# Kernel optimization log

Measured on AMD Instinct MI355X. Metric: run time of the kernel, lower is better.

Reference implementation:

```python
import jax, jax.numpy as jnp
import numpy as np

N = 8192          # num_points
RADIUS = 0.5


def _make_curve(num_points):
    # Reproduces the interp1d-based turbo-coil curve from __init__ (linear interp).
    xk = np.array([-2, -1, 0, 1, 1, 0, -1, -1, 0, 1, 2], dtype=np.float64)
    zk = np.array([0, 0, 1, 0, -1, 0, 1, 0, -1, 0, 0], dtype=np.float64)
    yk = np.array([0, 0, 1, 1, -1, -1, -1, 1, 1, 0, 0], dtype=np.float64)
    t = np.linspace(0.0, 1.0, len(xk))
    s = np.linspace(0.0, 1.0, num_points)
    return (np.interp(s, t, xk).astype(np.float32),
            np.interp(s, t, yk).astype(np.float32),
            np.interp(s, t, zk).astype(np.float32))


def setup_inputs() -> dict:
    x, y, z = _make_curve(N)
    return {"x": jnp.asarray(x), "y": jnp.asarray(y), "z": jnp.asarray(z)}


def _cdist(a, b):
    # pairwise Euclidean distance, safe at zero (subgradient 0 like torch.cdist)
    d2 = jnp.sum(a * a, -1, keepdims=True) - 2.0 * (a @ b.T) + jnp.sum(b * b, -1)
    d2 = jnp.maximum(d2, 0.0)
    safe = jnp.where(d2 > 0.0, d2, 1.0)
    return jnp.where(d2 > 0.0, jnp.sqrt(safe), 0.0)


def _mask_distances(dist, min_dist):
    # Original: for each row i, scan j = i, i+1, ... and overwrite entries with
    # min_dist+1 while dist[i,j] <= min_dist, breaking at the first entry that
    # exceeds min_dist (the j in range(i,0) loop is empty, so only the forward
    # scan matters). Vectorized: contiguous prefix-run starting at the diagonal.
    n = dist.shape[0]
    rows = jnp.arange(n)[:, None]
    cols = jnp.arange(n)[None, :]
    upper = cols >= rows
    cond = dist <= min_dist
    # cumprod along each row, seeded with 1 (True) left of the diagonal, so that
    # run[i,j] = all(cond[i, i..j]) for j >= i
    run = jnp.cumprod(jnp.where(upper, cond, True).astype(jnp.int32), axis=1)
    mask = upper & (run > 0)
    return jnp.where(mask, min_dist + 1.0, dist)


def _puffer_loss(p2d, low, high):
    # PufferZone(points_2d, -1.0, 1.0, x): out-of-bounds penalty on [low, high]
    return jax.nn.relu(p2d - high) + jax.nn.relu(low - p2d)


def _noise_loss(p2d):
    # noise_reduction_loss: penalize curvature (squared second differences)
    d2 = p2d[2:] - 2.0 * p2d[1:-1] + p2d[:-2]
    return d2 * d2


def reference(x, y, z, scale=1.0):
    p2d = jnp.stack([y, z], axis=1)          # [N, 2]
    p3d = jnp.stack([x, y, z], axis=1)       # [N, 3]

    fixed = _puffer_loss(p2d, -1.0, 1.0)

    dist = _cdist(p3d, p3d)                  # [N, N]
    min_dist = RADIUS * 2.0 * scale
    dist_mask = _mask_distances(dist, min_dist)
    intersect = jax.nn.relu(min_dist - dist_mask)

    noise = _noise_loss(p2d)

    # dist_loss (WeightedEuclideanDistance) taken as the pairwise cdist sum
    return (jnp.sum(fixed)
            + jnp.sum(dist) / 10000.0
            + jnp.sum(intersect)
            + jnp.sum(noise) * 10.0)
```

## Files before the change

### kernel.cpp

```cpp
#include <hip/hip_runtime.h>

constexpr int N = 8192;
constexpr float TRI = 33558528.0f;

__device__ __forceinline__ float fsqrt(float v) { return __builtin_amdgcn_sqrtf(v); }


__global__ __launch_bounds__(256)
void pack_kernel(const float* __restrict__ x, const float* __restrict__ y,
                 const float* __restrict__ z, float4* __restrict__ p4) {
    const int i = blockIdx.x * 256 + threadIdx.x;
    p4[i] = make_float4(x[i], y[i], z[i], 0.f);
}

__global__ __launch_bounds__(256, 8)
void main_kernel(const float4* __restrict__ p4,
                 float* __restrict__ row_sd, float* __restrict__ row_sm,
                 float* __restrict__ row_corr) {
    const int tid  = threadIdx.x;
    const int lane = tid & 63;
    const int wave = tid >> 6;

    if (blockIdx.x < 1024) {
        const int b       = blockIdx.x;
        const int topBase = 4 * b;
        const int botBase = N - 4 * (b + 1);

        float xr[8], yr[8], zr[8];
#pragma unroll
        for (int r = 0; r < 4; ++r) {
            const float4 pt = p4[topBase + r];
            const float4 pb = p4[botBase + r];
            xr[r]     = pt.x; yr[r]     = pt.y; zr[r]     = pt.z;
            xr[4 + r] = pb.x; yr[4 + r] = pb.y; zr[4 + r] = pb.z;
        }
        float sd[8], sm[8];
#pragma unroll
        for (int r = 0; r < 8; ++r) { sd[r] = 0.f; sm[r] = 0.f; }

#pragma unroll
        for (int g = 0; g < 2; ++g) {
            const int base = g ? botBase : topBase;
            const int ro   = g * 4;

            {
                const int    j  = base + tid;
                const int    jc = (j < N) ? j : (N - 1);
                const float4 p  = p4[jc];
#pragma unroll
                for (int r = 0; r < 4; ++r) {
                    const float dx = p.x - xr[ro + r], dy = p.y - yr[ro + r], dz = p.z - zr[ro + r];
                    const float d  = fsqrt(dx * dx + dy * dy + dz * dz);
                    if (j < N && tid >= r) { sd[ro + r] += d; sm[ro + r] += fminf(d, 1.f); }
                }
            }
            int j0 = base + 256;
            if (j0 + 256 <= N) {
                float4 p = p4[j0 + tid];
                while (true) {
                    const float4 c    = p;
                    const bool   more = (j0 + 512 <= N);
                    if (more) p = p4[j0 + 256 + tid];
#pragma unroll
                    for (int r = 0; r < 4; ++r) {
                        const float dx = c.x - xr[ro + r], dy = c.y - yr[ro + r], dz = c.z - zr[ro + r];
                        const float d  = fsqrt(dx * dx + dy * dy + dz * dz);
                        sd[ro + r] += d; sm[ro + r] += fminf(d, 1.f);
                    }
                    j0 += 256;
                    if (!more) break;
                }
            }
            if (j0 < N) {
                const int j = j0 + tid;
                if (j < N) {
                    const float4 p = p4[j];
#pragma unroll
                    for (int r = 0; r < 4; ++r) {
                        const float dx = p.x - xr[ro + r], dy = p.y - yr[ro + r], dz = p.z - zr[ro + r];
                        const float d  = fsqrt(dx * dx + dy * dy + dz * dz);
                        sd[ro + r] += d; sm[ro + r] += fminf(d, 1.f);
                    }
                }
            }
        }

        __shared__ float lsd[4][8];
        __shared__ float lsm[4][8];
#pragma unroll
        for (int r = 0; r < 8; ++r) {
            float a = sd[r], c = sm[r];
#pragma unroll
            for (int off = 32; off; off >>= 1) {
                a += __shfl_down(a, off);
                c += __shfl_down(c, off);
            }
            if (lane == 0) { lsd[wave][r] = a; lsm[wave][r] = c; }
        }
        __syncthreads();
        if (tid < 8) {
            const float a = lsd[0][tid] + lsd[1][tid] + lsd[2][tid] + lsd[3][tid];
            const float c = lsm[0][tid] + lsm[1][tid] + lsm[2][tid] + lsm[3][tid];
            const int   i = (tid < 4) ? (topBase + tid) : (botBase + tid - 4);
            row_sd[i] = a;
            row_sm[i] = c;
        }
    } else {
        const int cb = blockIdx.x - 1024;
#pragma unroll
        for (int rr = 0; rr < 2; ++rr) {
            const int    i  = 8 * cb + 2 * wave + rr;
            const float4 pi = p4[i];
            float corr = 0.f;
            int   jb   = i;
            float4 a  = p4[min(jb + lane,      N - 1)];
            float4 bq = p4[min(jb + 64 + lane, N - 1)];
            while (true) {
                const float4 na = p4[min(jb + 128 + lane, N - 1)];
                const float4 nb = p4[min(jb + 192 + lane, N - 1)];
                const int j0i = jb + lane, j1i = jb + 64 + lane;
                float dx = a.x - pi.x, dy = a.y - pi.y, dz = a.z - pi.z;
                const float d0 = fsqrt(dx * dx + dy * dy + dz * dz);
                dx = bq.x - pi.x; dy = bq.y - pi.y; dz = bq.z - pi.z;
                const float d1 = fsqrt(dx * dx + dy * dy + dz * dz);
                const unsigned long long m0 = __ballot(j0i >= N || d0 > 1.f);
                const unsigned long long m1 = __ballot(j1i >= N || d1 > 1.f);
                int stop;
                if (m0)      stop = __builtin_ctzll(m0);
                else if (m1) stop = 64 + __builtin_ctzll(m1);
                else         stop = 128;
                if (lane < stop)      corr += 1.f - d0;
                if (64 + lane < stop) corr += 1.f - d1;
                if (stop < 128) break;
                jb += 128;
                a = na; bq = nb;
            }
#pragma unroll
            for (int off = 32; off; off >>= 1) corr += __shfl_down(corr, off);
            if (lane == 0) row_corr[i] = corr;
        }
    }
}

__global__ __launch_bounds__(256)
void partial_kernel(const float* __restrict__ y, const float* __restrict__ z,
                    const float* __restrict__ row_sd, const float* __restrict__ row_sm,
                    const float* __restrict__ row_corr, float* __restrict__ partials) {
    const int tid = threadIdx.x;
    const int i   = blockIdx.x * 256 + tid;
    float v[5];
    v[0] = row_sd[i];
    v[1] = row_sm[i];
    v[2] = row_corr[i];
    const float yv = y[i], zv = z[i];
    v[3] = fmaxf(yv - 1.f, 0.f) + fmaxf(-1.f - yv, 0.f)
         + fmaxf(zv - 1.f, 0.f) + fmaxf(-1.f - zv, 0.f);
    v[4] = 0.f;
    if (i < N - 2) {
        const float d2y = y[i + 2] - 2.f * y[i + 1] + y[i];
        const float d2z = z[i + 2] - 2.f * z[i + 1] + z[i];
        v[4] = d2y * d2y + d2z * d2z;
    }
    const int lane = tid & 63, wave = tid >> 6;
    __shared__ float s[4][5];
#pragma unroll
    for (int c = 0; c < 5; ++c) {
        float a = v[c];
#pragma unroll
        for (int off = 32; off; off >>= 1) a += __shfl_down(a, off);
        if (lane == 0) s[wave][c] = a;
    }
    __syncthreads();
    if (tid == 0) {
#pragma unroll
        for (int c = 0; c < 5; ++c)
            partials[blockIdx.x * 5 + c] = s[0][c] + s[1][c] + s[2][c] + s[3][c];
    }
}

__global__ __launch_bounds__(64)
void final_kernel(const float* __restrict__ partials, float* __restrict__ out) {
    const int tid = threadIdx.x;
    float a[5] = {0.f, 0.f, 0.f, 0.f, 0.f};
    if (tid < 32) {
#pragma unroll
        for (int c = 0; c < 5; ++c) a[c] = partials[tid * 5 + c];
    }
#pragma unroll
    for (int c = 0; c < 5; ++c) {
#pragma unroll
        for (int off = 16; off; off >>= 1) a[c] += __shfl_down(a[c], off, 32);
    }
    if (tid == 0) {
        const float A = a[0], M = a[1], C = a[2], fix = a[3], noise = a[4];
        out[0] = fix + (2.f * A) / 10000.f
               + (2.f * (TRI - M) - (float)N - C) + 10.f * noise;
    }
}

extern "C" void kernel_launch(void* const* d_in, const int* in_sizes, int n_in,
                              void* d_out, int out_size, void* d_ws, size_t ws_size,
                              hipStream_t stream) {
    const float* x = (const float*)d_in[0];
    const float* y = (const float*)d_in[1];
    const float* z = (const float*)d_in[2];
    float* out      = (float*)d_out;
    float4* p4      = (float4*)d_ws;
    float* row_sd   = (float*)(p4 + N);
    float* row_sm   = row_sd + N;
    float* row_corr = row_sm + N;
    float* partials = row_corr + N;

    pack_kernel<<<N / 256, 256, 0, stream>>>(x, y, z, p4);
    main_kernel<<<2048, 256, 0, stream>>>(p4, row_sd, row_sm, row_corr);
    partial_kernel<<<32, 256, 0, stream>>>(y, z, row_sd, row_sm, row_corr, partials);
    final_kernel<<<1, 64, 0, stream>>>(partials, out);
}
```

Before: 29.26 us.

## Fuse final reductions into main kernel via last-block atomic counter

Moves the puffer and noise partial sums into the pack kernel. The final reduction now runs inside main_kernel, in whichever block is last to increment a global atomic counter, so the partial_kernel and final_kernel launches go away. The aim is to remove two kernel launches and their gaps. In exchange, every block does a fence and an atomic, and the last block serially reduces 3x8192 row values.

```diff
diff --git a/kernel.cpp b/kernel.cpp
--- a/kernel.cpp
+++ b/kernel.cpp
@@ -2,21 +2,49 @@
 
 constexpr int N = 8192;
 constexpr float TRI = 33558528.0f;
+constexpr int MAIN_BLOCKS = 2048;
 
 __device__ __forceinline__ float fsqrt(float v) { return __builtin_amdgcn_sqrtf(v); }
 
 
 __global__ __launch_bounds__(256)
 void pack_kernel(const float* __restrict__ x, const float* __restrict__ y,
-                 const float* __restrict__ z, float4* __restrict__ p4) {
-    const int i = blockIdx.x * 256 + threadIdx.x;
-    p4[i] = make_float4(x[i], y[i], z[i], 0.f);
+                 const float* __restrict__ z, float4* __restrict__ p4,
+                 float* __restrict__ partials, unsigned* __restrict__ counter) {
+    const int tid = threadIdx.x;
+    const int i   = blockIdx.x * 256 + tid;
+    if (i == 0) *counter = 0u;
+
+    const float yv = y[i], zv = z[i];
+    p4[i] = make_float4(x[i], yv, zv, 0.f);
+
+    float fix = fmaxf(yv - 1.f, 0.f) + fmaxf(-1.f - yv, 0.f)
+              + fmaxf(zv - 1.f, 0.f) + fmaxf(-1.f - zv, 0.f);
+    float noise = 0.f;
+    if (i < N - 2) {
+        const float d2y = y[i + 2] - 2.f * y[i + 1] + y[i];
+        const float d2z = z[i + 2] - 2.f * z[i + 1] + z[i];
+        noise = d2y * d2y + d2z * d2z;
+    }
+    const int lane = tid & 63, wave = tid >> 6;
+    __shared__ float s[4][2];
+    for (int off = 32; off; off >>= 1) {
+        fix   += __shfl_down(fix, off);
+        noise += __shfl_down(noise, off);
+    }
+    if (lane == 0) { s[wave][0] = fix; s[wave][1] = noise; }
+    __syncthreads();
+    if (tid == 0) {
+        partials[blockIdx.x * 2]     = s[0][0] + s[1][0] + s[2][0] + s[3][0];
+        partials[blockIdx.x * 2 + 1] = s[0][1] + s[1][1] + s[2][1] + s[3][1];
+    }
 }
 
 __global__ __launch_bounds__(256, 8)
 void main_kernel(const float4* __restrict__ p4,
                  float* __restrict__ row_sd, float* __restrict__ row_sm,
-                 float* __restrict__ row_corr) {
+                 float* __restrict__ row_corr, const float* __restrict__ partials,
+                 unsigned* __restrict__ counter, float* __restrict__ out) {
     const int tid  = threadIdx.x;
     const int lane = tid & 63;
     const int wave = tid >> 6;
@@ -140,61 +168,43 @@
             if (lane == 0) row_corr[i] = corr;
         }
     }
-}
-
-__global__ __launch_bounds__(256)
-void partial_kernel(const float* __restrict__ y, const float* __restrict__ z,
-                    const float* __restrict__ row_sd, const float* __restrict__ row_sm,
-                    const float* __restrict__ row_corr, float* __restrict__ partials) {
-    const int tid = threadIdx.x;
-    const int i   = blockIdx.x * 256 + tid;
-    float v[5];
-    v[0] = row_sd[i];
-    v[1] = row_sm[i];
-    v[2] = row_corr[i];
-    const float yv = y[i], zv = z[i];
-    v[3] = fmaxf(yv - 1.f, 0.f) + fmaxf(-1.f - yv, 0.f)
-         + fmaxf(zv - 1.f, 0.f) + fmaxf(-1.f - zv, 0.f);
-    v[4] = 0.f;
-    if (i < N - 2) {
-        const float d2y = y[i + 2] - 2.f * y[i + 1] + y[i];
-        const float d2z = z[i + 2] - 2.f * z[i + 1] + z[i];
-        v[4] = d2y * d2y + d2z * d2z;
-    }
-    const int lane = tid & 63, wave = tid >> 6;
-    __shared__ float s[4][5];
-#pragma unroll
-    for (int c = 0; c < 5; ++c) {
-        float a = v[c];
-#pragma unroll
-        for (int off = 32; off; off >>= 1) a += __shfl_down(a, off);
-        if (lane == 0) s[wave][c] = a;
-    }
+
+    __shared__ unsigned s_old;
     __syncthreads();
     if (tid == 0) {
-#pragma unroll
-        for (int c = 0; c < 5; ++c)
-            partials[blockIdx.x * 5 + c] = s[0][c] + s[1][c] + s[2][c] + s[3][c];
-    }
-}
-
-__global__ __launch_bounds__(64)
-void final_kernel(const float* __restrict__ partials, float* __restrict__ out) {
-    const int tid = threadIdx.x;
-    float a[5] = {0.f, 0.f, 0.f, 0.f, 0.f};
-    if (tid < 32) {
-#pragma unroll
-        for (int c = 0; c < 5; ++c) a[c] = partials[tid * 5 + c];
-    }
-#pragma unroll
-    for (int c = 0; c < 5; ++c) {
-#pragma unroll
-        for (int off = 16; off; off >>= 1) a[c] += __shfl_down(a[c], off, 32);
-    }
-    if (tid == 0) {
-        const float A = a[0], M = a[1], C = a[2], fix = a[3], noise = a[4];
-        out[0] = fix + (2.f * A) / 10000.f
-               + (2.f * (TRI - M) - (float)N - C) + 10.f * noise;
+        __threadfence();
+        s_old = atomicAdd(counter, 1u);
+    }
+    __syncthreads();
+    if (s_old == MAIN_BLOCKS - 1) {
+        __threadfence();
+        float A = 0.f, M = 0.f, C = 0.f;
+        for (int i = tid; i < N; i += 256) {
+            A += row_sd[i];
+            M += row_sm[i];
+            C += row_corr[i];
+        }
+        float fx = 0.f, nz = 0.f;
+        if (tid < 32) { fx = partials[tid * 2]; nz = partials[tid * 2 + 1]; }
+        __shared__ float s[4][5];
+        float v[5] = {A, M, C, fx, nz};
+#pragma unroll
+        for (int c = 0; c < 5; ++c) {
+#pragma unroll
+            for (int off = 32; off; off >>= 1) v[c] += __shfl_down(v[c], off);
+        }
+        if (lane == 0) {
+#pragma unroll
+            for (int c = 0; c < 5; ++c) s[wave][c] = v[c];
+        }
+        __syncthreads();
+        if (tid == 0) {
+            float t[5];
+#pragma unroll
+            for (int c = 0; c < 5; ++c) t[c] = s[0][c] + s[1][c] + s[2][c] + s[3][c];
+            out[0] = t[3] + (2.f * t[0]) / 10000.f
+                   + (2.f * (TRI - t[1]) - (float)N - t[2]) + 10.f * t[4];
+        }
     }
 }
 
@@ -210,9 +220,9 @@
     float* row_sm   = row_sd + N;
     float* row_corr = row_sm + N;
     float* partials = row_corr + N;
-
-    pack_kernel<<<N / 256, 256, 0, stream>>>(x, y, z, p4);
-    main_kernel<<<2048, 256, 0, stream>>>(p4, row_sd, row_sm, row_corr);
-    partial_kernel<<<32, 256, 0, stream>>>(y, z, row_sd, row_sm, row_corr, partials);
-    final_kernel<<<1, 64, 0, stream>>>(partials, out);
+    unsigned* counter = (unsigned*)(partials + 64);
+
+    pack_kernel<<<N / 256, 256, 0, stream>>>(x, y, z, p4, partials, counter);
+    main_kernel<<<MAIN_BLOCKS, 256, 0, stream>>>(p4, row_sd, row_sm, row_corr,
+                                                 partials, counter, out);
 }
```

Measured after the change: 73.68 us (median of 3 runs). +151.8%, slower.

## Stage point tiles into LDS with async global_load_lds double buffering

Applied to the files above, without the earlier changes.

The row-sum blocks now stream the point array through shared memory in 1024-point tiles, loaded with async global-to-LDS transfers and double buffered. Each tile is reused by both the top and bottom row groups instead of each scanning global memory separately. Per-element masking is applied only on the tiles that hold the diagonal starts. Occupancy drops to 4 blocks per SIMD bound because of the 32 KB LDS buffer, and a barrier is added per tile.

```diff
diff --git a/kernel.cpp b/kernel.cpp
--- a/kernel.cpp
+++ b/kernel.cpp
@@ -13,10 +13,11 @@
     p4[i] = make_float4(x[i], y[i], z[i], 0.f);
 }
 
-__global__ __launch_bounds__(256, 8)
+__global__ __launch_bounds__(256, 4)
 void main_kernel(const float4* __restrict__ p4,
                  float* __restrict__ row_sd, float* __restrict__ row_sm,
                  float* __restrict__ row_corr) {
+    __shared__ float4 buf[2][1024];
     const int tid  = threadIdx.x;
     const int lane = tid & 63;
     const int wave = tid >> 6;
@@ -38,51 +39,67 @@
 #pragma unroll
         for (int r = 0; r < 8; ++r) { sd[r] = 0.f; sm[r] = 0.f; }
 
-#pragma unroll
-        for (int g = 0; g < 2; ++g) {
-            const int base = g ? botBase : topBase;
-            const int ro   = g * 4;
-
-            {
-                const int    j  = base + tid;
-                const int    jc = (j < N) ? j : (N - 1);
-                const float4 p  = p4[jc];
-#pragma unroll
-                for (int r = 0; r < 4; ++r) {
-                    const float dx = p.x - xr[ro + r], dy = p.y - yr[ro + r], dz = p.z - zr[ro + r];
-                    const float d  = fsqrt(dx * dx + dy * dy + dz * dz);
-                    if (j < N && tid >= r) { sd[ro + r] += d; sm[ro + r] += fminf(d, 1.f); }
+        const int t0  = topBase >> 10;
+        const int tb0 = botBase >> 10;
+
+        auto stage = [&](int t, int s) {
+#pragma unroll
+            for (int q = 0; q < 4; ++q) {
+                __builtin_amdgcn_global_load_lds(
+                    (const __attribute__((address_space(1))) uint32_t*)(p4 + t * 1024 + q * 256 + tid),
+                    (__attribute__((address_space(3))) uint32_t*)(&buf[s][q * 256 + tid]),
+                    16, 0, 0);
+            }
+        };
+
+        int cur = 0;
+        stage(t0, 0);
+        __syncthreads();
+
+        for (int t = t0; t < 8; ++t) {
+            if (t < 7) stage(t + 1, cur ^ 1);
+            const int  tbase  = t << 10;
+            const bool hasBot = (t >= tb0);
+            const bool pred   = (t == t0) || (t == tb0);
+#pragma unroll
+            for (int it = 0; it < 4; ++it) {
+                const int    idx = (wave << 8) + (it << 6) + lane;
+                const float4 c   = buf[cur][idx];
+                const int    j   = tbase + idx;
+                if (pred) {
+#pragma unroll
+                    for (int r = 0; r < 4; ++r) {
+                        const float dx = c.x - xr[r], dy = c.y - yr[r], dz = c.z - zr[r];
+                        const float d  = fsqrt(dx * dx + dy * dy + dz * dz);
+                        if (j >= topBase + r) { sd[r] += d; sm[r] += fminf(d, 1.f); }
+                    }
+                    if (hasBot) {
+#pragma unroll
+                        for (int r = 0; r < 4; ++r) {
+                            const float dx = c.x - xr[4 + r], dy = c.y - yr[4 + r], dz = c.z - zr[4 + r];
+                            const float d  = fsqrt(dx * dx + dy * dy + dz * dz);
+                            if (j >= botBase + r) { sd[4 + r] += d; sm[4 + r] += fminf(d, 1.f); }
+                        }
+                    }
+                } else {
+#pragma unroll
+                    for (int r = 0; r < 4; ++r) {
+                        const float dx = c.x - xr[r], dy = c.y - yr[r], dz = c.z - zr[r];
+                        const float d  = fsqrt(dx * dx + dy * dy + dz * dz);
+                        sd[r] += d; sm[r] += fminf(d, 1.f);
+                    }
+                    if (hasBot) {
+#pragma unroll
+                        for (int r = 0; r < 4; ++r) {
+                            const float dx = c.x - xr[4 + r], dy = c.y - yr[4 + r], dz = c.z - zr[4 + r];
+                            const float d  = fsqrt(dx * dx + dy * dy + dz * dz);
+                            sd[4 + r] += d; sm[4 + r] += fminf(d, 1.f);
+                        }
+                    }
                 }
             }
-            int j0 = base + 256;
-            if (j0 + 256 <= N) {
-                float4 p = p4[j0 + tid];
-                while (true) {
-                    const float4 c    = p;
-                    const bool   more = (j0 + 512 <= N);
-                    if (more) p = p4[j0 + 256 + tid];
-#pragma unroll
-                    for (int r = 0; r < 4; ++r) {
-                        const float dx = c.x - xr[ro + r], dy = c.y - yr[ro + r], dz = c.z - zr[ro + r];
-                        const float d  = fsqrt(dx * dx + dy * dy + dz * dz);
-                        sd[ro + r] += d; sm[ro + r] += fminf(d, 1.f);
-                    }
-                    j0 += 256;
-                    if (!more) break;
-                }
-            }
-            if (j0 < N) {
-                const int j = j0 + tid;
-                if (j < N) {
-                    const float4 p = p4[j];
-#pragma unroll
-                    for (int r = 0; r < 4; ++r) {
-                        const float dx = p.x - xr[ro + r], dy = p.y - yr[ro + r], dz = p.z - zr[ro + r];
-                        const float d  = fsqrt(dx * dx + dy * dy + dz * dz);
-                        sd[ro + r] += d; sm[ro + r] += fminf(d, 1.f);
-                    }
-                }
-            }
+            __syncthreads();
+            cur ^= 1;
         }
 
         __shared__ float lsd[4][8];
```

Result: slower. 33.83 us (+15.6%).

## Merge top and bottom row scans into one aligned column sweep sharing loads

Applied to the files above, without the earlier changes.

The separate sweeps for the top and bottom row groups become a single loop over 256-aligned column chunks. Each loaded point is reused for both groups once the sweep reaches the bottom rows, which cuts global loads. Per-row query coordinates are forced into scalar registers via readfirstlane to free vector registers. In exchange, each iteration carries extra predication and branching, and the aligned start adds a partially wasted first chunk.

```diff
diff --git a/kernel.cpp b/kernel.cpp
--- a/kernel.cpp
+++ b/kernel.cpp
@@ -4,6 +4,9 @@
 constexpr float TRI = 33558528.0f;
 
 __device__ __forceinline__ float fsqrt(float v) { return __builtin_amdgcn_sqrtf(v); }
+__device__ __forceinline__ float sgpr(float v) {
+    return __int_as_float(__builtin_amdgcn_readfirstlane(__float_as_int(v)));
+}
 
 
 __global__ __launch_bounds__(256)
@@ -31,55 +34,51 @@
         for (int r = 0; r < 4; ++r) {
             const float4 pt = p4[topBase + r];
             const float4 pb = p4[botBase + r];
-            xr[r]     = pt.x; yr[r]     = pt.y; zr[r]     = pt.z;
-            xr[4 + r] = pb.x; yr[4 + r] = pb.y; zr[4 + r] = pb.z;
+            xr[r]     = sgpr(pt.x); yr[r]     = sgpr(pt.y); zr[r]     = sgpr(pt.z);
+            xr[4 + r] = sgpr(pb.x); yr[4 + r] = sgpr(pb.y); zr[4 + r] = sgpr(pb.z);
         }
         float sd[8], sm[8];
 #pragma unroll
         for (int r = 0; r < 8; ++r) { sd[r] = 0.f; sm[r] = 0.f; }
 
-#pragma unroll
-        for (int g = 0; g < 2; ++g) {
-            const int base = g ? botBase : topBase;
-            const int ro   = g * 4;
-
-            {
-                const int    j  = base + tid;
-                const int    jc = (j < N) ? j : (N - 1);
-                const float4 p  = p4[jc];
+        const int cstart = topBase & ~255;
+        float4 p = p4[cstart + tid];
+        for (int c = cstart; c < N; c += 256) {
+            const float4 cur = p;
+            if (c + 256 < N) p = p4[c + 256 + tid];
+            const int  j       = c + tid;
+            const bool botAct  = (c + 256 > botBase);
+            const bool topPred = (c < topBase + 4);
+            const bool botPred = botAct && (c < botBase + 4);
+
+            if (topPred || botPred) {
 #pragma unroll
                 for (int r = 0; r < 4; ++r) {
-                    const float dx = p.x - xr[ro + r], dy = p.y - yr[ro + r], dz = p.z - zr[ro + r];
+                    const float dx = cur.x - xr[r], dy = cur.y - yr[r], dz = cur.z - zr[r];
                     const float d  = fsqrt(dx * dx + dy * dy + dz * dz);
-                    if (j < N && tid >= r) { sd[ro + r] += d; sm[ro + r] += fminf(d, 1.f); }
-                }
-            }
-            int j0 = base + 256;
-            if (j0 + 256 <= N) {
-                float4 p = p4[j0 + tid];
-                while (true) {
-                    const float4 c    = p;
-                    const bool   more = (j0 + 512 <= N);
-                    if (more) p = p4[j0 + 256 + tid];
+                    if (j >= topBase + r) { sd[r] += d; sm[r] += fminf(d, 1.f); }
+                }
+                if (botAct) {
 #pragma unroll
                     for (int r = 0; r < 4; ++r) {
-                        const float dx = c.x - xr[ro + r], dy = c.y - yr[ro + r], dz = c.z - zr[ro + r];
+                        const float dx = cur.x - xr[4 + r], dy = cur.y - yr[4 + r], dz = cur.z - zr[4 + r];
                         const float d  = fsqrt(dx * dx + dy * dy + dz * dz);
-                        sd[ro + r] += d; sm[ro + r] += fminf(d, 1.f);
+                        if (j >= botBase + r) { sd[4 + r] += d; sm[4 + r] += fminf(d, 1.f); }
                     }
-                    j0 += 256;
-                    if (!more) break;
-                }
-            }
-            if (j0 < N) {
-                const int j = j0 + tid;
-                if (j < N) {
-                    const float4 p = p4[j];
+                }
+            } else {
+#pragma unroll
+                for (int r = 0; r < 4; ++r) {
+                    const float dx = cur.x - xr[r], dy = cur.y - yr[r], dz = cur.z - zr[r];
+                    const float d  = fsqrt(dx * dx + dy * dy + dz * dz);
+                    sd[r] += d; sm[r] += fminf(d, 1.f);
+                }
+                if (botAct) {
 #pragma unroll
                     for (int r = 0; r < 4; ++r) {
-                        const float dx = p.x - xr[ro + r], dy = p.y - yr[ro + r], dz = p.z - zr[ro + r];
+                        const float dx = cur.x - xr[4 + r], dy = cur.y - yr[4 + r], dz = cur.z - zr[4 + r];
                         const float d  = fsqrt(dx * dx + dy * dy + dz * dz);
-                        sd[ro + r] += d; sm[ro + r] += fminf(d, 1.f);
+                        sd[4 + r] += d; sm[4 + r] += fminf(d, 1.f);
                     }
                 }
             }
```

Result: slower. 31.14 us (+6.5%).
